# Optimization experiments

Measured on AMD Instinct MI355X. Metric: run time of the kernel, lower is better.

## Reference

```python
import jax, jax.numpy as jnp
import numpy as np
from jax import lax

# static config
P = 16          # patch_len
S = 8           # stride_base
MAX_OFF = 4.0


def setup_inputs() -> dict:
    key = jax.random.key(0)
    ks = jax.random.split(key, 7)
    B, L, N, A, D = 64, 512, 64, 64, 256
    x = jax.random.normal(ks[0], (B, L, N), dtype=jnp.float32)
    conv_w = jax.random.normal(ks[1], (32, N, 3), dtype=jnp.float32) * 0.05
    conv_b = jnp.zeros((32,), dtype=jnp.float32)
    lin_w = jax.random.normal(ks[2], (A, 32), dtype=jnp.float32) * 0.1
    lin_b = jnp.zeros((A,), dtype=jnp.float32)
    wp_w = jax.random.normal(ks[3], (D, P), dtype=jnp.float32) * 0.1
    wp_b = jnp.zeros((D,), dtype=jnp.float32)
    return {"x": x, "conv_w": conv_w, "conv_b": conv_b,
            "lin_w": lin_w, "lin_b": lin_b, "wp_w": wp_w, "wp_b": wp_b}


def _forward(x, conv_w, conv_b, lin_w, lin_b, wp_w, wp_b):
    B, L, N = x.shape
    A = lin_w.shape[0]
    D = wp_w.shape[0]
    z = jnp.transpose(x, (0, 2, 1))  # (B, N, L) -- channels = series

    # offset head: Conv1d(N->32, k=3, pad=1) -> ReLU -> global avg pool -> Linear(32->A)
    h = lax.conv_general_dilated(z, conv_w, window_strides=(1,),
                                 padding=[(1, 1)],
                                 dimension_numbers=("NCH", "OIH", "NCH"))
    h = jax.nn.relu(h + conv_b[None, :, None])      # (B, 32, L)
    pooled = jnp.mean(h, axis=-1)                    # (B, 32)
    delta = MAX_OFF * jnp.tanh(pooled @ lin_w.T + lin_b)  # (B, A)

    # sampling positions: anchor + offset + centered patch index, clamped to [0, L-1]
    anchors = jnp.arange(A, dtype=jnp.float32) * S
    pidx = jnp.arange(P, dtype=jnp.float32) - (P - 1) / 2.0
    xs = anchors[None, :, None] + delta[:, :, None] + pidx[None, None, :]  # (B, A, P)
    xs = jnp.clip(xs, 0.0, float(L - 1))

    # 1D bilinear gather (equivalent to grid_sample with y=0, border pad, align_corners=True)
    i0 = jnp.floor(xs).astype(jnp.int32)
    f = xs - i0.astype(xs.dtype)                     # (B, A, P)
    i1 = jnp.minimum(i0 + 1, L - 1)
    gather = jax.vmap(lambda zb, ib: zb[:, ib])      # (N,L),(A,P) -> (N,A,P)
    g0 = gather(z, i0)                               # (B, N, A, P)
    g1 = gather(z, i1)
    samp = g0 * (1.0 - f)[:, None] + g1 * f[:, None]  # (B, N, A, P)

    # patch projection W_P: (P -> D)
    out = jnp.einsum("bnap,dp->bnad", samp, wp_w) + wp_b  # (B, N, A, D)
    return out.reshape(B * N, A, D)


def reference(x, conv_w, conv_b, lin_w, lin_b, wp_w, wp_b):
    return _forward(x, conv_w, conv_b, lin_w, lin_b, wp_w, wp_b)
```

## Files before the change

kernel.cpp:

```cpp
#include <hip/hip_runtime.h>
#include <hip/hip_bf16.h>
#include <cmath>

#define BB 64
#define LL 512
#define NN 64
#define AA 64
#define PP 16
#define DD 256
#define MAX_OFF 4.0f
#define STRIDE_S 8

typedef __attribute__((ext_vector_type(8))) short short8_t;
typedef __attribute__((ext_vector_type(4))) float float4_t;

static __device__ __forceinline__ unsigned short f2bf(float x) {
    union { float f; unsigned u; } v; v.f = x;
    unsigned r = (v.u + 0x7FFFu + ((v.u >> 16) & 1u)) >> 16;
    return (unsigned short)r;
}

__global__ __launch_bounds__(256) void conv_pool_kernel(
    const float* __restrict__ x,
    const float* __restrict__ conv_w,
    const float* __restrict__ conv_b,
    float* __restrict__ pool_partial)
{
    const int c = blockIdx.x;
    const int b = blockIdx.y;
    const int t = threadIdx.x;

    __shared__ float4 wl[3 * 16 * 32];
    __shared__ float  xl[66 * 64];
    __shared__ float  red[8][32];

    for (int idx = t; idx < 1536; idx += 256) {
        int o  = idx & 31;
        int nv = (idx >> 5) & 15;
        int k  = idx >> 9;
        float4 v;
        v.x = conv_w[(o * 64 + nv * 4 + 0) * 3 + k];
        v.y = conv_w[(o * 64 + nv * 4 + 1) * 3 + k];
        v.z = conv_w[(o * 64 + nv * 4 + 2) * 3 + k];
        v.w = conv_w[(o * 64 + nv * 4 + 3) * 3 + k];
        wl[idx] = v;
    }

    const int base_row = c * 64 - 1;
    for (int idx = t; idx < 66 * 16; idx += 256) {
        int j  = idx >> 4;
        int nv = idx & 15;
        int row = base_row + j;
        float4 v = make_float4(0.f, 0.f, 0.f, 0.f);
        if (row >= 0 && row < LL)
            v = *reinterpret_cast<const float4*>(&x[((size_t)b * LL + row) * NN + nv * 4]);
        *reinterpret_cast<float4*>(&xl[j * 64 + nv * 4]) = v;
    }
    __syncthreads();

    const int o  = t & 31;
    const int lg = t >> 5;

    float s[8];
#pragma unroll
    for (int j = 0; j < 8; ++j) s[j] = 0.f;

#pragma unroll
    for (int nv = 0; nv < 16; ++nv) {
        float4 xv[10];
#pragma unroll
        for (int j = 0; j < 10; ++j)
            xv[j] = *reinterpret_cast<const float4*>(&xl[(lg * 8 + j) * 64 + nv * 4]);
#pragma unroll
        for (int k = 0; k < 3; ++k) {
            float4 w4 = wl[(k * 16 + nv) * 32 + o];
#pragma unroll
            for (int j = 0; j < 8; ++j) {
                s[j] = fmaf(xv[j + k].x, w4.x, s[j]);
                s[j] = fmaf(xv[j + k].y, w4.y, s[j]);
                s[j] = fmaf(xv[j + k].z, w4.z, s[j]);
                s[j] = fmaf(xv[j + k].w, w4.w, s[j]);
            }
        }
    }

    const float cb = conv_b[o];
    float part = 0.f;
#pragma unroll
    for (int j = 0; j < 8; ++j) part += fmaxf(s[j] + cb, 0.f);
    red[lg][o] = part;
    __syncthreads();

    if (t < 32) {
        float sum = 0.f;
#pragma unroll
        for (int g = 0; g < 8; ++g) sum += red[g][t];
        pool_partial[((size_t)b * 8 + c) * 32 + t] = sum;
    }
}

__global__ __launch_bounds__(64) void delta_kernel(
    const float* __restrict__ pool_partial,
    const float* __restrict__ lin_w,
    const float* __restrict__ lin_b,
    float* __restrict__ delta)
{
    const int b = blockIdx.x;
    const int t = threadIdx.x;
    __shared__ float pooled[32];

    if (t < 32) {
        float s = 0.f;
#pragma unroll
        for (int c = 0; c < 8; ++c) s += pool_partial[((size_t)b * 8 + c) * 32 + t];
        pooled[t] = s * (1.0f / 512.0f);
    }
    __syncthreads();

    float s = lin_b[t];
#pragma unroll
    for (int o = 0; o < 32; ++o) s = fmaf(pooled[o], lin_w[t * 32 + o], s);
    delta[b * AA + t] = MAX_OFF * tanhf(s);
}

#define XR_STRIDE 68
#define SA_STRIDE 40
#define BW_STRIDE 24

__global__ __launch_bounds__(256) void patch_proj_kernel(
    const float* __restrict__ x,
    const float* __restrict__ wp_w,
    const float* __restrict__ wp_b,
    const float* __restrict__ delta,
    float* __restrict__ out)
{
    const int a = blockIdx.x;
    const int b = blockIdx.y;
    const int t = threadIdx.x;
    const int lane = t & 63;
    const int w  = t >> 6;
    const int lg = lane >> 4;
    const int lr = lane & 15;

    __shared__ float          xr[17 * XR_STRIDE];
    __shared__ unsigned short sampA[64 * SA_STRIDE];
    __shared__ unsigned short bw[256 * BW_STRIDE];

    const float dlt  = delta[b * AA + a];
    const float base = (float)(a * STRIDE_S) - 7.5f + dlt;
    const int   r0   = (int)floorf(base);

    for (int idx = t; idx < 17 * 16; idx += 256) {
        int j  = idx >> 4;
        int nv = idx & 15;
        int row = max(0, min(LL - 1, r0 + j));
        float4 v = *reinterpret_cast<const float4*>(&x[((size_t)b * LL + row) * NN + nv * 4]);
        *reinterpret_cast<float4*>(&xr[j * XR_STRIDE + nv * 4]) = v;
    }
    for (int idx = t; idx < 256 * 8; idx += 256) {
        int d  = idx >> 3;
        int pp = idx & 7;
        float2 v = *reinterpret_cast<const float2*>(&wp_w[d * 16 + pp * 2]);
        unsigned pk = (unsigned)f2bf(v.x) | ((unsigned)f2bf(v.y) << 16);
        *reinterpret_cast<unsigned*>(&bw[d * BW_STRIDE + pp * 2]) = pk;
    }
    for (int idx = t; idx < 64 * 8; idx += 256) {
        int n  = idx >> 3;
        int ww = idx & 7;
        reinterpret_cast<unsigned*>(&sampA[n * SA_STRIDE])[8 + ww] = 0u;
    }
    __syncthreads();

    {
        const int pp  = t & 7;
        const int nr0 = t >> 3;
        float f_[2]; int j0_[2], j1_[2];
#pragma unroll
        for (int q = 0; q < 2; ++q) {
            int p = pp * 2 + q;
            float xs = base + (float)p;
            xs = fminf(fmaxf(xs, 0.f), (float)(LL - 1));
            int i0 = (int)floorf(xs);
            f_[q]  = xs - (float)i0;
            j0_[q] = i0 - r0;
            j1_[q] = min(i0 + 1, LL - 1) - r0;
        }
#pragma unroll
        for (int h = 0; h < 2; ++h) {
            int n = nr0 + 32 * h;
            unsigned pk = 0;
#pragma unroll
            for (int q = 0; q < 2; ++q) {
                float g0 = xr[j0_[q] * XR_STRIDE + n];
                float g1 = xr[j1_[q] * XR_STRIDE + n];
                float s  = g0 + f_[q] * (g1 - g0);
                pk |= (unsigned)f2bf(s) << (16 * q);
            }
            *reinterpret_cast<unsigned*>(&sampA[n * SA_STRIDE + pp * 2]) = pk;
        }
    }

    short8_t bfrag[4];
    float4_t acc[4][4];
#pragma unroll
    for (int i = 0; i < 4; ++i) {
        int d = (w * 4 + i) * 16 + lr;
        bfrag[i] = *reinterpret_cast<const short8_t*>(&bw[d * BW_STRIDE + (lg & 1) * 8]);
        float bias = wp_b[d];
        float4_t c4 = {bias, bias, bias, bias};
#pragma unroll
        for (int s = 0; s < 4; ++s) acc[s][i] = c4;
    }
    __syncthreads();

    short8_t afrag[4];
#pragma unroll
    for (int s = 0; s < 4; ++s)
        afrag[s] = *reinterpret_cast<const short8_t*>(
            &sampA[(s * 16 + lr) * SA_STRIDE + lg * 8]);

#pragma unroll
    for (int s = 0; s < 4; ++s)
#pragma unroll
        for (int i = 0; i < 4; ++i)
            acc[s][i] = __builtin_amdgcn_mfma_f32_16x16x32_bf16(
                afrag[s], bfrag[i], acc[s][i], 0, 0, 0);

    const size_t obase = ((size_t)(b * NN) * AA + a) * DD + (size_t)w * 64 + lr;
#pragma unroll
    for (int s = 0; s < 4; ++s) {
#pragma unroll
        for (int j = 0; j < 4; ++j) {
            const int n = s * 16 + lg * 4 + j;
            const size_t rowoff = obase + (size_t)n * (AA * DD);
#pragma unroll
            for (int i = 0; i < 4; ++i)
                out[rowoff + i * 16] = acc[s][i][j];
        }
    }
}

extern "C" void kernel_launch(void* const* d_in, const int* in_sizes, int n_in,
                              void* d_out, int out_size, void* d_ws, size_t ws_size,
                              hipStream_t stream)
{
    const float* x      = (const float*)d_in[0];
    const float* conv_w = (const float*)d_in[1];
    const float* conv_b = (const float*)d_in[2];
    const float* lin_w  = (const float*)d_in[3];
    const float* lin_b  = (const float*)d_in[4];
    const float* wp_w   = (const float*)d_in[5];
    const float* wp_b   = (const float*)d_in[6];
    float* out = (float*)d_out;

    float* pool_partial = (float*)d_ws;
    float* delta        = pool_partial + 16384;

    conv_pool_kernel<<<dim3(8, BB), 256, 0, stream>>>(x, conv_w, conv_b, pool_partial);
    delta_kernel<<<BB, 64, 0, stream>>>(pool_partial, lin_w, lin_b, delta);
    patch_proj_kernel<<<dim3(AA, BB), 256, 0, stream>>>(x, wp_w, wp_b, delta, out);
}
```

Baseline: 66.47 us.

## Pre-convert patch weights to bf16 once and swap MFMA operands for vector stores

```diff
diff --git a/kernel.cpp b/kernel.cpp
--- a/kernel.cpp
+++ b/kernel.cpp
@@ -14,10 +14,9 @@
 typedef __attribute__((ext_vector_type(8))) short short8_t;
 typedef __attribute__((ext_vector_type(4))) float float4_t;
 
-static __device__ __forceinline__ unsigned short f2bf(float x) {
+static __device__ __forceinline__ unsigned f2bf(float x) {
     union { float f; unsigned u; } v; v.f = x;
-    unsigned r = (v.u + 0x7FFFu + ((v.u >> 16) & 1u)) >> 16;
-    return (unsigned short)r;
+    return (v.u + 0x7FFFu + ((v.u >> 16) & 1u)) >> 16;
 }
 
 __global__ __launch_bounds__(256) void conv_pool_kernel(
@@ -103,7 +102,9 @@
     const float* __restrict__ pool_partial,
     const float* __restrict__ lin_w,
     const float* __restrict__ lin_b,
-    float* __restrict__ delta)
+    const float* __restrict__ wp_w,
+    float* __restrict__ delta,
+    unsigned short* __restrict__ wp16)
 {
     const int b = blockIdx.x;
     const int t = threadIdx.x;
@@ -121,15 +122,27 @@
 #pragma unroll
     for (int o = 0; o < 32; ++o) s = fmaf(pooled[o], lin_w[t * 32 + o], s);
     delta[b * AA + t] = MAX_OFF * tanhf(s);
+
+    if (b == 0) {
+        const float4* w4 = reinterpret_cast<const float4*>(wp_w);
+        uint2* o2 = reinterpret_cast<uint2*>(wp16);
+#pragma unroll
+        for (int i = 0; i < 16; ++i) {
+            float4 v = w4[i * 64 + t];
+            uint2 pk;
+            pk.x = f2bf(v.x) | (f2bf(v.y) << 16);
+            pk.y = f2bf(v.z) | (f2bf(v.w) << 16);
+            o2[i * 64 + t] = pk;
+        }
+    }
 }
 
 #define XR_STRIDE 68
-#define SA_STRIDE 40
-#define BW_STRIDE 24
+#define SA_ST     24
 
 __global__ __launch_bounds__(256) void patch_proj_kernel(
     const float* __restrict__ x,
-    const float* __restrict__ wp_w,
+    const unsigned short* __restrict__ wp16,
     const float* __restrict__ wp_b,
     const float* __restrict__ delta,
     float* __restrict__ out)
@@ -143,8 +156,7 @@
     const int lr = lane & 15;
 
     __shared__ float          xr[17 * XR_STRIDE];
-    __shared__ unsigned short sampA[64 * SA_STRIDE];
-    __shared__ unsigned short bw[256 * BW_STRIDE];
+    __shared__ unsigned short sampA[64 * SA_ST];
 
     const float dlt  = delta[b * AA + a];
     const float base = (float)(a * STRIDE_S) - 7.5f + dlt;
@@ -157,17 +169,19 @@
         float4 v = *reinterpret_cast<const float4*>(&x[((size_t)b * LL + row) * NN + nv * 4]);
         *reinterpret_cast<float4*>(&xr[j * XR_STRIDE + nv * 4]) = v;
     }
-    for (int idx = t; idx < 256 * 8; idx += 256) {
-        int d  = idx >> 3;
-        int pp = idx & 7;
-        float2 v = *reinterpret_cast<const float2*>(&wp_w[d * 16 + pp * 2]);
-        unsigned pk = (unsigned)f2bf(v.x) | ((unsigned)f2bf(v.y) << 16);
-        *reinterpret_cast<unsigned*>(&bw[d * BW_STRIDE + pp * 2]) = pk;
-    }
-    for (int idx = t; idx < 64 * 8; idx += 256) {
-        int n  = idx >> 3;
-        int ww = idx & 7;
-        reinterpret_cast<unsigned*>(&sampA[n * SA_STRIDE])[8 + ww] = 0u;
+
+    short8_t afrag[4];
+    float4_t acc[4][4];
+    const short8_t zero8 = {0, 0, 0, 0, 0, 0, 0, 0};
+#pragma unroll
+    for (int i = 0; i < 4; ++i) {
+        const int d = w * 64 + i * 16 + lr;
+        short8_t v = *reinterpret_cast<const short8_t*>(&wp16[d * 16 + (lg & 1) * 8]);
+        afrag[i] = (lg < 2) ? v : zero8;
+        float4 bv = *reinterpret_cast<const float4*>(&wp_b[w * 64 + i * 16 + lg * 4]);
+        float4_t c4 = {bv.x, bv.y, bv.z, bv.w};
+#pragma unroll
+        for (int s = 0; s < 4; ++s) acc[s][i] = c4;
     }
     __syncthreads();
 
@@ -194,49 +208,34 @@
                 float g0 = xr[j0_[q] * XR_STRIDE + n];
                 float g1 = xr[j1_[q] * XR_STRIDE + n];
                 float s  = g0 + f_[q] * (g1 - g0);
-                pk |= (unsigned)f2bf(s) << (16 * q);
+                pk |= f2bf(s) << (16 * q);
             }
-            *reinterpret_cast<unsigned*>(&sampA[n * SA_STRIDE + pp * 2]) = pk;
-        }
-    }
+            *reinterpret_cast<unsigned*>(&sampA[n * SA_ST + pp * 2]) = pk;
+        }
+    }
+    __syncthreads();
 
     short8_t bfrag[4];
-    float4_t acc[4][4];
-#pragma unroll
-    for (int i = 0; i < 4; ++i) {
-        int d = (w * 4 + i) * 16 + lr;
-        bfrag[i] = *reinterpret_cast<const short8_t*>(&bw[d * BW_STRIDE + (lg & 1) * 8]);
-        float bias = wp_b[d];
-        float4_t c4 = {bias, bias, bias, bias};
-#pragma unroll
-        for (int s = 0; s < 4; ++s) acc[s][i] = c4;
-    }
-    __syncthreads();
-
-    short8_t afrag[4];
 #pragma unroll
     for (int s = 0; s < 4; ++s)
-        afrag[s] = *reinterpret_cast<const short8_t*>(
-            &sampA[(s * 16 + lr) * SA_STRIDE + lg * 8]);
+        bfrag[s] = *reinterpret_cast<const short8_t*>(
+            &sampA[(s * 16 + lr) * SA_ST + (lg & 1) * 8]);
 
 #pragma unroll
     for (int s = 0; s < 4; ++s)
 #pragma unroll
         for (int i = 0; i < 4; ++i)
             acc[s][i] = __builtin_amdgcn_mfma_f32_16x16x32_bf16(
-                afrag[s], bfrag[i], acc[s][i], 0, 0, 0);
-
-    const size_t obase = ((size_t)(b * NN) * AA + a) * DD + (size_t)w * 64 + lr;
+                afrag[i], bfrag[s], acc[s][i], 0, 0, 0);
+
+    const size_t ob = (((size_t)b * NN) * AA + a) * DD + w * 64 + lg * 4;
 #pragma unroll
     for (int s = 0; s < 4; ++s) {
-#pragma unroll
-        for (int j = 0; j < 4; ++j) {
-            const int n = s * 16 + lg * 4 + j;
-            const size_t rowoff = obase + (size_t)n * (AA * DD);
-#pragma unroll
-            for (int i = 0; i < 4; ++i)
-                out[rowoff + i * 16] = acc[s][i][j];
-        }
+        const int n = s * 16 + lr;
+        const size_t rb = ob + (size_t)n * (AA * DD);
+#pragma unroll
+        for (int i = 0; i < 4; ++i)
+            *reinterpret_cast<float4_t*>(&out[rb + i * 16]) = acc[s][i];
     }
 }
 
@@ -255,8 +254,9 @@
 
     float* pool_partial = (float*)d_ws;
     float* delta        = pool_partial + 16384;
+    unsigned short* wp16 = (unsigned short*)(delta + 4096);
 
     conv_pool_kernel<<<dim3(8, BB), 256, 0, stream>>>(x, conv_w, conv_b, pool_partial);
-    delta_kernel<<<BB, 64, 0, stream>>>(pool_partial, lin_w, lin_b, delta);
-    patch_proj_kernel<<<dim3(AA, BB), 256, 0, stream>>>(x, wp_w, wp_b, delta, out);
-}
+    delta_kernel<<<BB, 64, 0, stream>>>(pool_partial, lin_w, lin_b, wp_w, delta, wp16);
+    patch_proj_kernel<<<dim3(AA, BB), 256, 0, stream>>>(x, wp16, wp_b, delta, out);
+}
```

Result: no change. 65.52 us, median of 2 (-1.4%).
